# Kernel tuning notes

Measured on AMD Instinct MI355X. Metric: run time of the kernel, lower is better.

Reference implementation:

```python
import jax, jax.numpy as jnp
import numpy as np

B, H, W = 8, 1024, 1024
IN_DIM, HID, OUT_DIM = 8, 16, 3


def setup_inputs() -> dict:
    key = jax.random.key(0)
    ks = jax.random.split(key, 8)
    x = jax.random.uniform(ks[0], (B, H, W, IN_DIM), dtype=jnp.float32)
    mask = jax.random.randint(ks[1], (B, H, W), 0, 2).astype(jnp.bool_)
    # kaiming-uniform-ish hidden weights, xavier-ish last layer, zero biases
    w0 = jax.random.uniform(ks[2], (IN_DIM, HID), jnp.float32, -1.0, 1.0) * np.sqrt(6.0 / IN_DIM)
    b0 = jnp.zeros((HID,), jnp.float32)
    w1 = jax.random.uniform(ks[3], (HID, HID), jnp.float32, -1.0, 1.0) * np.sqrt(6.0 / HID)
    b1 = jnp.zeros((HID,), jnp.float32)
    w2 = jax.random.uniform(ks[4], (HID, OUT_DIM), jnp.float32, -1.0, 1.0) * np.sqrt(6.0 / (HID + OUT_DIM))
    b2 = jnp.zeros((OUT_DIM,), jnp.float32)
    return {"x": x, "mask": mask, "w0": w0, "b0": b0, "w1": w1, "b1": b1, "w2": w2, "b2": b2}


def reference(x, mask, w0, b0, w1, b1, w2, b2):
    # x: [B,H,W,IN_DIM]; mask: [B,H,W] bool
    rgb = x[..., :3]            # [B,H,W,3]
    res = x[..., 3:4]           # [B,H,W,1]
    # tiny 2-hidden-layer MLP with ReLU, sigmoid head (dense; masked rows zeroed after)
    h = jax.nn.relu(jnp.einsum('bhwi,ij->bhwj', x, w0) + b0)
    h = jax.nn.relu(jnp.einsum('bhwi,ij->bhwj', h, w1) + b1)
    y = jax.nn.sigmoid(jnp.einsum('bhwi,ij->bhwj', h, w2) + b2)  # [B,H,W,3]
    blended = (1.0 - res) * rgb + res * y
    # masked-out pixels are exactly zero, matching the torch scatter into zeros
    return jnp.where(mask[..., None], blended, jnp.zeros((), x.dtype))
```

## Files before the change

### kernel.cpp

```cpp
#include <hip/hip_runtime.h>

#define NPIX (8 * 1024 * 1024)
#define IN 8
#define HID 16
#define OUTC 3
#define BLK 256
#define PPT 2

#define WS_W0T 16
#define WS_W1T 144
#define WS_W2T 400
#define WS_B0  448
#define WS_B1  464
#define WS_B2  480

__global__ void prep_kernel(const unsigned int* __restrict__ m,
                            const float* __restrict__ w0, const float* __restrict__ b0,
                            const float* __restrict__ w1, const float* __restrict__ b1,
                            const float* __restrict__ w2, const float* __restrict__ b2,
                            float* __restrict__ ws) {
    const int t = threadIdx.x;
    if (t < 64) {
        unsigned int acc = 0u;
        #pragma unroll
        for (int k = 0; k < 8; ++k) acc |= m[t * 8 + k];
        const unsigned long long big = __ballot(acc > 1u);
        if (t == 0) ((int*)ws)[0] = big ? 1 : 0;
    }
    if (t < HID * IN)  { int j = t >> 3, i = t & 7;   ws[WS_W0T + j * IN  + i] = w0[i * HID  + j]; }
    {                    int j = t >> 4, i = t & 15;  ws[WS_W1T + j * HID + i] = w1[i * HID  + j]; }
    if (t < OUTC * HID){ int j = t >> 4, i = t & 15;  ws[WS_W2T + j * HID + i] = w2[i * OUTC + j]; }
    if (t < HID)  { ws[WS_B0 + t] = b0[t]; ws[WS_B1 + t] = b1[t]; }
    if (t < OUTC) { ws[WS_B2 + t] = b2[t]; }
}

__global__ void __launch_bounds__(BLK) colormlp_kernel(
    const float* __restrict__ x,
    const void*  __restrict__ mask,
    const float* __restrict__ ws,
    float* __restrict__ out)
{
    __shared__ __align__(16) float sOut[BLK * PPT * OUTC];

    const int t = threadIdx.x;
    const int mflag = ((const int*)ws)[0];

    const unsigned int pix0 = (blockIdx.x * BLK + t) * PPT;

    float4 x0[PPT], x1[PPT];
    {
        const float4* xp = (const float4*)(x + (size_t)pix0 * IN);
        #pragma unroll
        for (int p = 0; p < PPT; ++p) { x0[p] = xp[2 * p]; x1[p] = xp[2 * p + 1]; }
    }

    float h0[PPT][HID];
    #pragma unroll
    for (int j = 0; j < HID; ++j) {
        const float* wr = ws + WS_W0T + j * IN;
        float w[IN];
        #pragma unroll
        for (int i = 0; i < IN; ++i) w[i] = wr[i];
        const float bj = ws[WS_B0 + j];
        #pragma unroll
        for (int p = 0; p < PPT; ++p) {
            float acc = bj;
            acc = fmaf(x0[p].x, w[0], acc);
            acc = fmaf(x0[p].y, w[1], acc);
            acc = fmaf(x0[p].z, w[2], acc);
            acc = fmaf(x0[p].w, w[3], acc);
            acc = fmaf(x1[p].x, w[4], acc);
            acc = fmaf(x1[p].y, w[5], acc);
            acc = fmaf(x1[p].z, w[6], acc);
            acc = fmaf(x1[p].w, w[7], acc);
            h0[p][j] = fmaxf(acc, 0.0f);
        }
    }
    __builtin_amdgcn_sched_barrier(0);

    float h1[PPT][HID];
    #pragma unroll
    for (int j = 0; j < HID; ++j) {
        const float* wr = ws + WS_W1T + j * HID;
        float w[HID];
        #pragma unroll
        for (int i = 0; i < HID; ++i) w[i] = wr[i];
        const float bj = ws[WS_B1 + j];
        #pragma unroll
        for (int p = 0; p < PPT; ++p) {
            float acc = bj;
            #pragma unroll
            for (int i = 0; i < HID; ++i) acc = fmaf(h0[p][i], w[i], acc);
            h1[p][j] = fmaxf(acc, 0.0f);
        }
    }
    __builtin_amdgcn_sched_barrier(0);

    int mv[PPT];
    if (mflag) {
        uchar2 m2 = *(const uchar2*)((const unsigned char*)mask + pix0);
        mv[0] = m2.x; mv[1] = m2.y;
    } else {
        int2 m2 = *(const int2*)((const int*)mask + pix0);
        mv[0] = m2.x; mv[1] = m2.y;
    }

    #pragma unroll
    for (int p = 0; p < PPT; ++p) {
        const float res = x0[p].w;
        float ov[OUTC];
        #pragma unroll
        for (int j = 0; j < OUTC; ++j) {
            const float* wr = ws + WS_W2T + j * HID;
            float acc = ws[WS_B2 + j];
            #pragma unroll
            for (int i = 0; i < HID; ++i) acc = fmaf(h1[p][i], wr[i], acc);
            float e = __expf(-acc);
            float y = __builtin_amdgcn_rcpf(1.0f + e);
            float rgb = (j == 0) ? x0[p].x : (j == 1) ? x0[p].y : x0[p].z;
            float bl = fmaf(res, y - rgb, rgb);
            ov[j] = mv[p] ? bl : 0.0f;
        }
        float* sp = sOut + (size_t)(t * PPT + p) * OUTC;
        ((float2*)sp)[0] = make_float2(ov[0], ov[1]);
        sp[2] = ov[2];
    }
    __syncthreads();

    {
        const float4* s4 = (const float4*)sOut;
        float4* o4 = (float4*)(out + (size_t)blockIdx.x * (BLK * PPT * OUTC));
        o4[t] = s4[t];
        if (t < (BLK * PPT * OUTC) / 4 - BLK) o4[BLK + t] = s4[BLK + t];
    }
}

extern "C" void kernel_launch(void* const* d_in, const int* in_sizes, int n_in,
                              void* d_out, int out_size, void* d_ws, size_t ws_size,
                              hipStream_t stream) {
    const float* x    = (const float*)d_in[0];
    const void*  mask = d_in[1];
    const float* w0   = (const float*)d_in[2];
    const float* b0   = (const float*)d_in[3];
    const float* w1   = (const float*)d_in[4];
    const float* b1   = (const float*)d_in[5];
    const float* w2   = (const float*)d_in[6];
    const float* b2   = (const float*)d_in[7];
    float* out = (float*)d_out;
    float* ws  = (float*)d_ws;

    prep_kernel<<<1, BLK, 0, stream>>>((const unsigned int*)mask,
                                       w0, b0, w1, b1, w2, b2, ws);

    const int grid = NPIX / (BLK * PPT);
    colormlp_kernel<<<grid, BLK, 0, stream>>>(x, mask, ws, out);
}
```

Baseline: 498.2 us.

## Use packed fp16 dot products for MLP layers with fp16 weights

Converts the inputs and hidden activations to packed fp16 and computes each layer with v_dot2 fp32-accumulate instructions. Weights are pre-packed as fp16 pairs in the workspace. This is meant to halve the FMA instruction count and the scalar weight loads. It trades accuracy for speed, since inputs are rounded to fp16, and it also adjusts launch bounds and drops the scheduling barriers.

```diff
diff --git a/kernel.cpp b/kernel.cpp
--- a/kernel.cpp
+++ b/kernel.cpp
@@ -7,12 +7,25 @@
 #define BLK 256
 #define PPT 2
 
-#define WS_W0T 16
-#define WS_W1T 144
-#define WS_W2T 400
-#define WS_B0  448
-#define WS_B1  464
-#define WS_B2  480
+typedef _Float16 f16x2 __attribute__((ext_vector_type(2)));
+
+__device__ __forceinline__ f16x2 pkrtz(float lo, float hi) {
+    return __builtin_bit_cast(f16x2, __builtin_amdgcn_cvt_pkrtz(lo, hi));
+}
+
+#define WS_W0H 16
+#define WS_W1H 80
+#define WS_W2H 208
+#define WS_B0  240
+#define WS_B1  256
+#define WS_B2  272
+
+__device__ __forceinline__ unsigned int pack2(float lo, float hi) {
+    _Float16 a = (_Float16)lo, b = (_Float16)hi;
+    unsigned short ua = __builtin_bit_cast(unsigned short, a);
+    unsigned short ub = __builtin_bit_cast(unsigned short, b);
+    return (unsigned int)ua | ((unsigned int)ub << 16);
+}
 
 __global__ void prep_kernel(const unsigned int* __restrict__ m,
                             const float* __restrict__ w0, const float* __restrict__ b0,
@@ -20,6 +33,7 @@
                             const float* __restrict__ w2, const float* __restrict__ b2,
                             float* __restrict__ ws) {
     const int t = threadIdx.x;
+    unsigned int* wsu = (unsigned int*)ws;
     if (t < 64) {
         unsigned int acc = 0u;
         #pragma unroll
@@ -27,14 +41,17 @@
         const unsigned long long big = __ballot(acc > 1u);
         if (t == 0) ((int*)ws)[0] = big ? 1 : 0;
     }
-    if (t < HID * IN)  { int j = t >> 3, i = t & 7;   ws[WS_W0T + j * IN  + i] = w0[i * HID  + j]; }
-    {                    int j = t >> 4, i = t & 15;  ws[WS_W1T + j * HID + i] = w1[i * HID  + j]; }
-    if (t < OUTC * HID){ int j = t >> 4, i = t & 15;  ws[WS_W2T + j * HID + i] = w2[i * OUTC + j]; }
+    if (t < 64)  { int j = t >> 2, k = t & 3;
+        wsu[WS_W0H + j * 4 + k] = pack2(w0[(2 * k) * HID + j], w0[(2 * k + 1) * HID + j]); }
+    if (t < 128) { int j = t >> 3, k = t & 7;
+        wsu[WS_W1H + j * 8 + k] = pack2(w1[(2 * k) * HID + j], w1[(2 * k + 1) * HID + j]); }
+    if (t < 24)  { int j = t >> 3, k = t & 7;
+        wsu[WS_W2H + j * 8 + k] = pack2(w2[(2 * k) * OUTC + j], w2[(2 * k + 1) * OUTC + j]); }
     if (t < HID)  { ws[WS_B0 + t] = b0[t]; ws[WS_B1 + t] = b1[t]; }
     if (t < OUTC) { ws[WS_B2 + t] = b2[t]; }
 }
 
-__global__ void __launch_bounds__(BLK) colormlp_kernel(
+__global__ void __launch_bounds__(BLK, 2) colormlp_kernel(
     const float* __restrict__ x,
     const void*  __restrict__ mask,
     const float* __restrict__ ws,
@@ -43,6 +60,7 @@
     __shared__ __align__(16) float sOut[BLK * PPT * OUTC];
 
     const int t = threadIdx.x;
+    const unsigned int* wsu = (const unsigned int*)ws;
     const int mflag = ((const int*)ws)[0];
 
     const unsigned int pix0 = (blockIdx.x * BLK + t) * PPT;
@@ -54,47 +72,62 @@
         for (int p = 0; p < PPT; ++p) { x0[p] = xp[2 * p]; x1[p] = xp[2 * p + 1]; }
     }
 
-    float h0[PPT][HID];
+    f16x2 xh[PPT][4];
     #pragma unroll
-    for (int j = 0; j < HID; ++j) {
-        const float* wr = ws + WS_W0T + j * IN;
-        float w[IN];
+    for (int p = 0; p < PPT; ++p) {
+        xh[p][0] = pkrtz(x0[p].x, x0[p].y);
+        xh[p][1] = pkrtz(x0[p].z, x0[p].w);
+        xh[p][2] = pkrtz(x1[p].x, x1[p].y);
+        xh[p][3] = pkrtz(x1[p].z, x1[p].w);
+    }
+
+    f16x2 h0h[PPT][HID / 2];
+    {
+        float h0[PPT][HID];
         #pragma unroll
-        for (int i = 0; i < IN; ++i) w[i] = wr[i];
-        const float bj = ws[WS_B0 + j];
+        for (int j = 0; j < HID; ++j) {
+            f16x2 w[4];
+            #pragma unroll
+            for (int k = 0; k < 4; ++k) w[k] = __builtin_bit_cast(f16x2, wsu[WS_W0H + j * 4 + k]);
+            const float bj = ws[WS_B0 + j];
+            #pragma unroll
+            for (int p = 0; p < PPT; ++p) {
+                float acc = bj;
+                #pragma unroll
+                for (int k = 0; k < 4; ++k) acc = __builtin_amdgcn_fdot2(xh[p][k], w[k], acc, false);
+                h0[p][j] = fmaxf(acc, 0.0f);
+            }
+        }
         #pragma unroll
-        for (int p = 0; p < PPT; ++p) {
-            float acc = bj;
-            acc = fmaf(x0[p].x, w[0], acc);
-            acc = fmaf(x0[p].y, w[1], acc);
-            acc = fmaf(x0[p].z, w[2], acc);
-            acc = fmaf(x0[p].w, w[3], acc);
-            acc = fmaf(x1[p].x, w[4], acc);
-            acc = fmaf(x1[p].y, w[5], acc);
-            acc = fmaf(x1[p].z, w[6], acc);
-            acc = fmaf(x1[p].w, w[7], acc);
-            h0[p][j] = fmaxf(acc, 0.0f);
+        for (int p = 0; p < PPT; ++p)
+            #pragma unroll
+            for (int i = 0; i < HID / 2; ++i)
+                h0h[p][i] = pkrtz(h0[p][2 * i], h0[p][2 * i + 1]);
+    }
+
+    f16x2 h1h[PPT][HID / 2];
+    {
+        float h1[PPT][HID];
+        #pragma unroll
+        for (int j = 0; j < HID; ++j) {
+            f16x2 w[8];
+            #pragma unroll
+            for (int k = 0; k < 8; ++k) w[k] = __builtin_bit_cast(f16x2, wsu[WS_W1H + j * 8 + k]);
+            const float bj = ws[WS_B1 + j];
+            #pragma unroll
+            for (int p = 0; p < PPT; ++p) {
+                float acc = bj;
+                #pragma unroll
+                for (int k = 0; k < 8; ++k) acc = __builtin_amdgcn_fdot2(h0h[p][k], w[k], acc, false);
+                h1[p][j] = fmaxf(acc, 0.0f);
+            }
         }
+        #pragma unroll
+        for (int p = 0; p < PPT; ++p)
+            #pragma unroll
+            for (int i = 0; i < HID / 2; ++i)
+                h1h[p][i] = pkrtz(h1[p][2 * i], h1[p][2 * i + 1]);
     }
-    __builtin_amdgcn_sched_barrier(0);
-
-    float h1[PPT][HID];
-    #pragma unroll
-    for (int j = 0; j < HID; ++j) {
-        const float* wr = ws + WS_W1T + j * HID;
-        float w[HID];
-        #pragma unroll
-        for (int i = 0; i < HID; ++i) w[i] = wr[i];
-        const float bj = ws[WS_B1 + j];
-        #pragma unroll
-        for (int p = 0; p < PPT; ++p) {
-            float acc = bj;
-            #pragma unroll
-            for (int i = 0; i < HID; ++i) acc = fmaf(h0[p][i], w[i], acc);
-            h1[p][j] = fmaxf(acc, 0.0f);
-        }
-    }
-    __builtin_amdgcn_sched_barrier(0);
 
     int mv[PPT];
     if (mflag) {
@@ -111,10 +144,11 @@
         float ov[OUTC];
         #pragma unroll
         for (int j = 0; j < OUTC; ++j) {
-            const float* wr = ws + WS_W2T + j * HID;
             float acc = ws[WS_B2 + j];
             #pragma unroll
-            for (int i = 0; i < HID; ++i) acc = fmaf(h1[p][i], wr[i], acc);
+            for (int k = 0; k < 8; ++k)
+                acc = __builtin_amdgcn_fdot2(h1h[p][k],
+                        __builtin_bit_cast(f16x2, wsu[WS_W2H + j * 8 + k]), acc, false);
             float e = __expf(-acc);
             float y = __builtin_amdgcn_rcpf(1.0f + e);
             float rgb = (j == 0) ? x0[p].x : (j == 1) ? x0[p].y : x0[p].z;
```

After: 431.5 us. 1.15x faster.

## Compute MLP layers with fp16 MFMA 16x16x16 instead of scalar FMAs

Applied to the files above, without the earlier changes.

Replaces per-thread fp32 FMA loops with three chained MFMA f16 instructions per 16-pixel chunk, with weights prepacked as fp16 A-fragments and biases used as the accumulator init. Each wave processes 8 chunks of 16 pixels in a loop, and lanes beyond 32 feed zeros for the padded K dimension. This removes most VALU work, at the cost of fp16 precision (round-toward-zero conversion) and narrower per-lane loads.

```diff
diff --git a/kernel.cpp b/kernel.cpp
--- a/kernel.cpp
+++ b/kernel.cpp
@@ -5,14 +5,34 @@
 #define HID 16
 #define OUTC 3
 #define BLK 256
-#define PPT 2
+#define CHAINS 8
+#define PXB (4 * CHAINS * 16)
 
-#define WS_W0T 16
-#define WS_W1T 144
-#define WS_W2T 400
-#define WS_B0  448
-#define WS_B1  464
-#define WS_B2  480
+typedef __fp16 f16x2 __attribute__((ext_vector_type(2)));
+typedef __fp16 f16x4 __attribute__((ext_vector_type(4)));
+typedef float  f32x4 __attribute__((ext_vector_type(4)));
+
+__device__ __forceinline__ f16x4 mk4(float a, float b, float c, float d) {
+    f16x2 p0 = __builtin_amdgcn_cvt_pkrtz(a, b);
+    f16x2 p1 = __builtin_amdgcn_cvt_pkrtz(c, d);
+    uint2 u = make_uint2(__builtin_bit_cast(unsigned int, p0),
+                         __builtin_bit_cast(unsigned int, p1));
+    return __builtin_bit_cast(f16x4, u);
+}
+
+#define WS_A0 16
+#define WS_A1 144
+#define WS_A2 272
+#define WS_B0 400
+#define WS_B1 416
+#define WS_B2 432
+
+__device__ __forceinline__ unsigned int pack2(float lo, float hi) {
+    __fp16 a = (__fp16)lo, b = (__fp16)hi;
+    unsigned short ua = __builtin_bit_cast(unsigned short, a);
+    unsigned short ub = __builtin_bit_cast(unsigned short, b);
+    return (unsigned int)ua | ((unsigned int)ub << 16);
+}
 
 __global__ void prep_kernel(const unsigned int* __restrict__ m,
                             const float* __restrict__ w0, const float* __restrict__ b0,
@@ -20,6 +40,7 @@
                             const float* __restrict__ w2, const float* __restrict__ b2,
                             float* __restrict__ ws) {
     const int t = threadIdx.x;
+    unsigned int* wsu = (unsigned int*)ws;
     if (t < 64) {
         unsigned int acc = 0u;
         #pragma unroll
@@ -27,111 +48,88 @@
         const unsigned long long big = __ballot(acc > 1u);
         if (t == 0) ((int*)ws)[0] = big ? 1 : 0;
     }
-    if (t < HID * IN)  { int j = t >> 3, i = t & 7;   ws[WS_W0T + j * IN  + i] = w0[i * HID  + j]; }
-    {                    int j = t >> 4, i = t & 15;  ws[WS_W1T + j * HID + i] = w1[i * HID  + j]; }
-    if (t < OUTC * HID){ int j = t >> 4, i = t & 15;  ws[WS_W2T + j * HID + i] = w2[i * OUTC + j]; }
-    if (t < HID)  { ws[WS_B0 + t] = b0[t]; ws[WS_B1 + t] = b1[t]; }
-    if (t < OUTC) { ws[WS_B2 + t] = b2[t]; }
+    if (t < 128) {
+        const int l = t >> 1, j = t & 1;
+        const int mcol = l & 15;
+        const int k0 = ((l >> 4) << 2) + 2 * j;
+        const float a0lo = (k0     < IN) ? w0[(k0    ) * HID + mcol] : 0.0f;
+        const float a0hi = (k0 + 1 < IN) ? w0[(k0 + 1) * HID + mcol] : 0.0f;
+        wsu[WS_A0 + t] = pack2(a0lo, a0hi);
+        wsu[WS_A1 + t] = pack2(w1[k0 * HID + mcol], w1[(k0 + 1) * HID + mcol]);
+        wsu[WS_A2 + t] = (mcol < OUTC)
+                       ? pack2(w2[k0 * OUTC + mcol], w2[(k0 + 1) * OUTC + mcol]) : 0u;
+    }
+    if (t < 16) {
+        ws[WS_B0 + t] = b0[t];
+        ws[WS_B1 + t] = b1[t];
+        ws[WS_B2 + t] = (t < OUTC) ? b2[t] : 0.0f;
+    }
 }
 
-__global__ void __launch_bounds__(BLK) colormlp_kernel(
+__global__ void __launch_bounds__(BLK, 4) colormlp_kernel(
     const float* __restrict__ x,
     const void*  __restrict__ mask,
     const float* __restrict__ ws,
     float* __restrict__ out)
 {
-    __shared__ __align__(16) float sOut[BLK * PPT * OUTC];
+    __shared__ __align__(16) float sOut[PXB * OUTC];
 
     const int t = threadIdx.x;
+    const int w = t >> 6;
+    const int l = t & 63;
+    const unsigned int* wsu = (const unsigned int*)ws;
     const int mflag = ((const int*)ws)[0];
 
-    const unsigned int pix0 = (blockIdx.x * BLK + t) * PPT;
+    const f16x4 a0 = __builtin_bit_cast(f16x4, *(const uint2*)&wsu[WS_A0 + 2 * l]);
+    const f16x4 a1 = __builtin_bit_cast(f16x4, *(const uint2*)&wsu[WS_A1 + 2 * l]);
+    const f16x4 a2 = __builtin_bit_cast(f16x4, *(const uint2*)&wsu[WS_A2 + 2 * l]);
 
-    float4 x0[PPT], x1[PPT];
-    {
-        const float4* xp = (const float4*)(x + (size_t)pix0 * IN);
-        #pragma unroll
-        for (int p = 0; p < PPT; ++p) { x0[p] = xp[2 * p]; x1[p] = xp[2 * p + 1]; }
-    }
+    const int g4 = (l >> 4) << 2;
+    const f32x4 cb0 = *(const f32x4*)&ws[WS_B0 + g4];
+    const f32x4 cb1 = *(const f32x4*)&ws[WS_B1 + g4];
+    const f32x4 cb2 = *(const f32x4*)&ws[WS_B2 + g4];
 
-    float h0[PPT][HID];
-    #pragma unroll
-    for (int j = 0; j < HID; ++j) {
-        const float* wr = ws + WS_W0T + j * IN;
-        float w[IN];
-        #pragma unroll
-        for (int i = 0; i < IN; ++i) w[i] = wr[i];
-        const float bj = ws[WS_B0 + j];
-        #pragma unroll
-        for (int p = 0; p < PPT; ++p) {
-            float acc = bj;
-            acc = fmaf(x0[p].x, w[0], acc);
-            acc = fmaf(x0[p].y, w[1], acc);
-            acc = fmaf(x0[p].z, w[2], acc);
-            acc = fmaf(x0[p].w, w[3], acc);
-            acc = fmaf(x1[p].x, w[4], acc);
-            acc = fmaf(x1[p].y, w[5], acc);
-            acc = fmaf(x1[p].z, w[6], acc);
-            acc = fmaf(x1[p].w, w[7], acc);
-            h0[p][j] = fmaxf(acc, 0.0f);
+    const unsigned int wavebase = (blockIdx.x * 4 + w) * (CHAINS * 16);
+
+    #pragma unroll 2
+    for (int c = 0; c < CHAINS; ++c) {
+        const unsigned int px = wavebase + c * 16 + (l & 15);
+
+        float4 xv = make_float4(0.f, 0.f, 0.f, 0.f);
+        if (l < 32) xv = ((const float4*)x)[(size_t)px * 2 + (l >> 4)];
+
+        f16x4 bf = mk4(xv.x, xv.y, xv.z, xv.w);
+        f32x4 d = __builtin_amdgcn_mfma_f32_16x16x16f16(a0, bf, cb0, 0, 0, 0);
+        bf = mk4(fmaxf(d[0], 0.f), fmaxf(d[1], 0.f), fmaxf(d[2], 0.f), fmaxf(d[3], 0.f));
+        d = __builtin_amdgcn_mfma_f32_16x16x16f16(a1, bf, cb1, 0, 0, 0);
+        bf = mk4(fmaxf(d[0], 0.f), fmaxf(d[1], 0.f), fmaxf(d[2], 0.f), fmaxf(d[3], 0.f));
+        d = __builtin_amdgcn_mfma_f32_16x16x16f16(a2, bf, cb2, 0, 0, 0);
+
+        if (l < 16) {
+            const int mv = mflag ? (int)((const unsigned char*)mask)[px]
+                                 : ((const int*)mask)[px];
+            const float res = xv.w;
+            float ov[OUTC];
+            #pragma unroll
+            for (int i = 0; i < OUTC; ++i) {
+                const float e = __expf(-d[i]);
+                const float y = __builtin_amdgcn_rcpf(1.0f + e);
+                const float rgb = (i == 0) ? xv.x : (i == 1) ? xv.y : xv.z;
+                const float bl = fmaf(res, y - rgb, rgb);
+                ov[i] = mv ? bl : 0.0f;
+            }
+            float* sp = sOut + (size_t)((w * CHAINS + c) * 16 + (l & 15)) * OUTC;
+            ((float2*)sp)[0] = make_float2(ov[0], ov[1]);
+            sp[2] = ov[2];
         }
-    }
-    __builtin_amdgcn_sched_barrier(0);
-
-    float h1[PPT][HID];
-    #pragma unroll
-    for (int j = 0; j < HID; ++j) {
-        const float* wr = ws + WS_W1T + j * HID;
-        float w[HID];
-        #pragma unroll
-        for (int i = 0; i < HID; ++i) w[i] = wr[i];
-        const float bj = ws[WS_B1 + j];
-        #pragma unroll
-        for (int p = 0; p < PPT; ++p) {
-            float acc = bj;
-            #pragma unroll
-            for (int i = 0; i < HID; ++i) acc = fmaf(h0[p][i], w[i], acc);
-            h1[p][j] = fmaxf(acc, 0.0f);
-        }
-    }
-    __builtin_amdgcn_sched_barrier(0);
-
-    int mv[PPT];
-    if (mflag) {
-        uchar2 m2 = *(const uchar2*)((const unsigned char*)mask + pix0);
-        mv[0] = m2.x; mv[1] = m2.y;
-    } else {
-        int2 m2 = *(const int2*)((const int*)mask + pix0);
-        mv[0] = m2.x; mv[1] = m2.y;
-    }
-
-    #pragma unroll
-    for (int p = 0; p < PPT; ++p) {
-        const float res = x0[p].w;
-        float ov[OUTC];
-        #pragma unroll
-        for (int j = 0; j < OUTC; ++j) {
-            const float* wr = ws + WS_W2T + j * HID;
-            float acc = ws[WS_B2 + j];
-            #pragma unroll
-            for (int i = 0; i < HID; ++i) acc = fmaf(h1[p][i], wr[i], acc);
-            float e = __expf(-acc);
-            float y = __builtin_amdgcn_rcpf(1.0f + e);
-            float rgb = (j == 0) ? x0[p].x : (j == 1) ? x0[p].y : x0[p].z;
-            float bl = fmaf(res, y - rgb, rgb);
-            ov[j] = mv[p] ? bl : 0.0f;
-        }
-        float* sp = sOut + (size_t)(t * PPT + p) * OUTC;
-        ((float2*)sp)[0] = make_float2(ov[0], ov[1]);
-        sp[2] = ov[2];
     }
     __syncthreads();
 
     {
         const float4* s4 = (const float4*)sOut;
-        float4* o4 = (float4*)(out + (size_t)blockIdx.x * (BLK * PPT * OUTC));
+        float4* o4 = (float4*)(out + (size_t)blockIdx.x * (PXB * OUTC));
         o4[t] = s4[t];
-        if (t < (BLK * PPT * OUTC) / 4 - BLK) o4[BLK + t] = s4[BLK + t];
+        if (t < (PXB * OUTC) / 4 - BLK) o4[BLK + t] = s4[BLK + t];
     }
 }
 
@@ -152,6 +150,6 @@
     prep_kernel<<<1, BLK, 0, stream>>>((const unsigned int*)mask,
                                        w0, b0, w1, b1, w2, b2, ws);
 
-    const int grid = NPIX / (BLK * PPT);
+    const int grid = NPIX / PXB;
     colormlp_kernel<<<grid, BLK, 0, stream>>>(x, mask, ws, out);
 }
```

New measurement: 436.0 us. 1.14x faster.
